# Optimization experiments

Hardware: AMD Instinct MI355X
Metric: run time of the kernel (lower is better)

The kernel has to match this reference:

```python
import jax, jax.numpy as jnp
import numpy as np

EPS = 1e-6          # AllReduceParams.eps for the fused RMSNorm
FP8_MAX = 448.0     # max finite magnitude of float8_e4m3fn


def setup_inputs() -> dict:
    key = jax.random.key(0)
    k1, k2, k3 = jax.random.split(key, 3)
    tp, T, H = 4, 4096, 8192  # tp ranks, tokens, hidden
    return {
        "input": jax.random.normal(k1, (tp, T, H), jnp.float32) * 0.05,
        "residual": jax.random.normal(k2, (T, H), jnp.float32),
        "norm_weight": jax.random.uniform(k3, (H,), jnp.float32, 0.5, 1.5),
        "scale": jnp.ones((1,), jnp.float32),  # static per-tensor FP8 scale
    }


def _fp8_e4m3_roundtrip(x):
    # Emulate e4m3 rounding; straight-through so the op stays differentiable.
    x = jnp.clip(x, -FP8_MAX, FP8_MAX)
    rounded = x.astype(jnp.float8_e4m3fn).astype(jnp.float32)
    return x + jax.lax.stop_gradient(rounded - x)


def reference(input, residual, norm_weight, scale):
    # All-reduce (sum over TP ranks) -- leading axis models the TP group.
    reduced = jnp.sum(input, axis=0)                 # [T, H]
    # Fused residual add.
    residual_out = reduced + residual                # [T, H]
    # Fused RMSNorm.
    var = jnp.mean(jnp.square(residual_out), axis=-1, keepdims=True)
    norm = residual_out * jax.lax.rsqrt(var + EPS) * norm_weight
    # Fused static per-tensor FP8 (e4m3) quantization: q = round_fp8(x * scale).
    quant = _fp8_e4m3_roundtrip(norm * scale)        # [T, H] fp8-rounded values
    return (quant, residual_out)
```

## Files before the change

### kernel.cpp

```cpp
#include <hip/hip_runtime.h>

constexpr int TP  = 4;
constexpr int TT  = 4096;
constexpr int HH  = 8192;
constexpr int BLK = 1024;
constexpr int NJ  = HH / (BLK * 4);

typedef float f32x4 __attribute__((ext_vector_type(4)));

__device__ __forceinline__ unsigned swz(unsigned byte) {
    return byte ^ (((byte >> 9) & 7u) << 4);
}

__device__ __forceinline__ double fp8_rne_d(double x) {
    long long b = (long long)__double_as_longlong(fabs(x));
    int ee = (int)(b >> 52);
    if (ee < 1017) ee = 1017;
    long long se = (long long)(ee - 3);
    double step = __longlong_as_double(se << 52);
    double inv  = __longlong_as_double((2046 - se) << 52);
    return rint(x * inv) * step;
}

__global__ __launch_bounds__(BLK, 8) void fused_ar_rms_fp8(
    const float* __restrict__ input,
    const float* __restrict__ residual,
    const float* __restrict__ weight,
    const float* __restrict__ scale,
    float* __restrict__ quant,
    float* __restrict__ resid_out)
{
    __shared__ float lds[HH];
    __shared__ float sred[8];

    const int t   = blockIdx.x;
    const int tid = threadIdx.x;
    const size_t row   = (size_t)t * HH;
    const size_t plane = (size_t)TT * HH;

    const f32x4* i0 = (const f32x4*)(input + row);
    const f32x4* i1 = (const f32x4*)(input + plane + row);
    const f32x4* i2 = (const f32x4*)(input + 2 * plane + row);
    const f32x4* i3 = (const f32x4*)(input + 3 * plane + row);
    const f32x4* rr = (const f32x4*)(residual + row);
    f32x4* qo = (f32x4*)(quant + row);
    f32x4* ro = (f32x4*)(resid_out + row);
    const f32x4* wv = (const f32x4*)weight;

    float s[NJ * 4];

    #pragma unroll
    for (int j = 0; j < NJ; ++j) {
        const int idx = j * BLK + tid;
        f32x4 a = i0[idx];
        f32x4 b = i1[idx];
        f32x4 c = i2[idx];
        f32x4 d = i3[idx];
        f32x4 r = rr[idx];
        f32x4 sv;
        #pragma unroll
        for (int k = 0; k < 4; ++k) {
            float v = __fadd_rn(a[k], b[k]);
            v = __fadd_rn(v, c[k]);
            v = __fadd_rn(v, d[k]);
            v = __fadd_rn(v, r[k]);
            sv[k] = v;
            s[j * 4 + k] = v;
        }
        *(f32x4*)((char*)lds + swz(16u * (unsigned)idx)) = sv;
        ro[idx] = sv;
    }
    __syncthreads();

    if (tid < 512) {
        const int leaf = tid >> 3;
        const int acc  = tid & 7;
        const unsigned base = (unsigned)(leaf * 512 + acc * 4);
        const char* lp = (const char*)lds;

        float x = *(const float*)(lp + swz(base));
        float r = __fmul_rn(x, x);
        #pragma unroll
        for (int i = 1; i < 16; ++i) {
            x = *(const float*)(lp + swz(base + 32u * i));
            r = __fadd_rn(r, __fmul_rn(x, x));
        }
        r = __fadd_rn(r, __shfl_xor(r, 1, 64));
        r = __fadd_rn(r, __shfl_xor(r, 2, 64));
        r = __fadd_rn(r, __shfl_xor(r, 4, 64));
        r = __fadd_rn(r, __shfl_xor(r, 8, 64));
        r = __fadd_rn(r, __shfl_xor(r, 16, 64));
        r = __fadd_rn(r, __shfl_xor(r, 32, 64));
        if ((tid & 63) == 0) sred[tid >> 6] = r;
    }
    __syncthreads();

    float p0 = sred[0], p1 = sred[1], p2 = sred[2], p3 = sred[3];
    float p4 = sred[4], p5 = sred[5], p6 = sred[6], p7 = sred[7];
    float res = __fadd_rn(
        __fadd_rn(__fadd_rn(p0, p1), __fadd_rn(p2, p3)),
        __fadd_rn(__fadd_rn(p4, p5), __fadd_rn(p6, p7)));
    const float mean = __fmul_rn(res, 1.0f / 8192.0f);
    const float vv   = __fadd_rn(mean, 1e-6f);
    const float rinv = __fdiv_rn(1.0f, __fsqrt_rn(vv));
    const float sc   = scale[0];

    #pragma unroll
    for (int j = 0; j < NJ; ++j) {
        const int idx = j * BLK + tid;
        f32x4 w4 = wv[idx];
        f32x4 qv;
        #pragma unroll
        for (int k = 0; k < 4; ++k) {
            float n = __fmul_rn(s[j * 4 + k], rinv);
            n = __fmul_rn(n, w4[k]);
            n = __fmul_rn(n, sc);
            n = fminf(fmaxf(n, -448.0f), 448.0f);
            qv[k] = (float)fp8_rne_d((double)n);
        }
        qo[idx] = qv;
    }
}

extern "C" void kernel_launch(void* const* d_in, const int* in_sizes, int n_in,
                              void* d_out, int out_size, void* d_ws, size_t ws_size,
                              hipStream_t stream) {
    const float* input    = (const float*)d_in[0];
    const float* residual = (const float*)d_in[1];
    const float* weight   = (const float*)d_in[2];
    const float* scale    = (const float*)d_in[3];
    float* quant     = (float*)d_out;
    float* resid_out = (float*)d_out + (size_t)TT * HH;

    fused_ar_rms_fp8<<<TT, BLK, 0, stream>>>(input, residual, weight, scale,
                                             quant, resid_out);
}
```

Measured before the change: 183.4 us.

## Shrink blocks to 256 threads, use all waves in reduction, float FP8 rounding

Cuts the block size from 1024 to 256 threads, so each thread holds 32 row values in registers instead of 8. The sum-of-squares reduction is restructured so all four waves take part, each lane accumulating two interleaved streams. The double-precision FP8 rounding is replaced by a float bit-manipulation version (integer round-to-nearest-even on the mantissa, plus a fixed-step path for subnormals), which avoids slow FP64 math. The larger per-thread register footprint and the new launch bound may limit occupancy on this bandwidth-bound kernel.

```diff
diff --git a/kernel.cpp b/kernel.cpp
--- a/kernel.cpp
+++ b/kernel.cpp
@@ -3,7 +3,7 @@
 constexpr int TP  = 4;
 constexpr int TT  = 4096;
 constexpr int HH  = 8192;
-constexpr int BLK = 1024;
+constexpr int BLK = 256;
 constexpr int NJ  = HH / (BLK * 4);
 
 typedef float f32x4 __attribute__((ext_vector_type(4)));
@@ -12,17 +12,14 @@
     return byte ^ (((byte >> 9) & 7u) << 4);
 }
 
-__device__ __forceinline__ double fp8_rne_d(double x) {
-    long long b = (long long)__double_as_longlong(fabs(x));
-    int ee = (int)(b >> 52);
-    if (ee < 1017) ee = 1017;
-    long long se = (long long)(ee - 3);
-    double step = __longlong_as_double(se << 52);
-    double inv  = __longlong_as_double((2046 - se) << 52);
-    return rint(x * inv) * step;
+__device__ __forceinline__ float fp8_rne_f(float n) {
+    unsigned u = __float_as_uint(n);
+    unsigned un = (u + 0x7FFFFu + ((u >> 20) & 1u)) & 0xFFF00000u;
+    float qs = rintf(__fmul_rn(n, 512.0f)) * (1.0f / 512.0f);
+    return ((u & 0x7FFFFFFFu) >= 0x3C800000u) ? __uint_as_float(un) : qs;
 }
 
-__global__ __launch_bounds__(BLK, 8) void fused_ar_rms_fp8(
+__global__ __launch_bounds__(BLK, 5) void fused_ar_rms_fp8(
     const float* __restrict__ input,
     const float* __restrict__ residual,
     const float* __restrict__ weight,
@@ -31,7 +28,7 @@
     float* __restrict__ resid_out)
 {
     __shared__ float lds[HH];
-    __shared__ float sred[8];
+    __shared__ float sred[4];
 
     const int t   = blockIdx.x;
     const int tid = threadIdx.x;
@@ -72,34 +69,39 @@
     }
     __syncthreads();
 
-    if (tid < 512) {
-        const int leaf = tid >> 3;
-        const int acc  = tid & 7;
-        const unsigned base = (unsigned)(leaf * 512 + acc * 4);
+    {
+        const int wave = tid >> 6;
+        const int lane = tid & 63;
+        const int leaf = wave * 16 + (lane >> 2);
+        const unsigned baseL = (unsigned)(leaf * 512 + (lane & 3) * 4);
         const char* lp = (const char*)lds;
 
-        float x = *(const float*)(lp + swz(base));
-        float r = __fmul_rn(x, x);
+        float xl = *(const float*)(lp + swz(baseL));
+        float xh = *(const float*)(lp + swz(baseL + 16));
+        float rL = __fmul_rn(xl, xl);
+        float rH = __fmul_rn(xh, xh);
         #pragma unroll
         for (int i = 1; i < 16; ++i) {
-            x = *(const float*)(lp + swz(base + 32u * i));
-            r = __fadd_rn(r, __fmul_rn(x, x));
+            xl = *(const float*)(lp + swz(baseL + 32u * i));
+            xh = *(const float*)(lp + swz(baseL + 32u * i + 16));
+            rL = __fadd_rn(rL, __fmul_rn(xl, xl));
+            rH = __fadd_rn(rH, __fmul_rn(xh, xh));
         }
-        r = __fadd_rn(r, __shfl_xor(r, 1, 64));
-        r = __fadd_rn(r, __shfl_xor(r, 2, 64));
+        rL = __fadd_rn(rL, __shfl_xor(rL, 1, 64));
+        rL = __fadd_rn(rL, __shfl_xor(rL, 2, 64));
+        rH = __fadd_rn(rH, __shfl_xor(rH, 1, 64));
+        rH = __fadd_rn(rH, __shfl_xor(rH, 2, 64));
+        float r = __fadd_rn(rL, rH);
         r = __fadd_rn(r, __shfl_xor(r, 4, 64));
         r = __fadd_rn(r, __shfl_xor(r, 8, 64));
         r = __fadd_rn(r, __shfl_xor(r, 16, 64));
         r = __fadd_rn(r, __shfl_xor(r, 32, 64));
-        if ((tid & 63) == 0) sred[tid >> 6] = r;
+        if (lane == 0) sred[wave] = r;
     }
     __syncthreads();
 
-    float p0 = sred[0], p1 = sred[1], p2 = sred[2], p3 = sred[3];
-    float p4 = sred[4], p5 = sred[5], p6 = sred[6], p7 = sred[7];
-    float res = __fadd_rn(
-        __fadd_rn(__fadd_rn(p0, p1), __fadd_rn(p2, p3)),
-        __fadd_rn(__fadd_rn(p4, p5), __fadd_rn(p6, p7)));
+    const float res = __fadd_rn(__fadd_rn(sred[0], sred[1]),
+                                __fadd_rn(sred[2], sred[3]));
     const float mean = __fmul_rn(res, 1.0f / 8192.0f);
     const float vv   = __fadd_rn(mean, 1e-6f);
     const float rinv = __fdiv_rn(1.0f, __fsqrt_rn(vv));
@@ -116,7 +118,7 @@
             n = __fmul_rn(n, w4[k]);
             n = __fmul_rn(n, sc);
             n = fminf(fmaxf(n, -448.0f), 448.0f);
-            qv[k] = (float)fp8_rne_d((double)n);
+            qv[k] = fp8_rne_f(n);
         }
         qo[idx] = qv;
     }
```

Measured after the change: 181.6 us. Within noise of the previous version (-1.0%).
